# Kernel optimization log

Measured on AMD Instinct MI355X. Metric: run time of the kernel, lower is better.

## Reference

```python
import jax, jax.numpy as jnp
import numpy as np

N0, N1, N2, DEG = 100000, 50000, 25000, 16
IN, HID, OUT = 256, 128, 128
H1, H2 = 2, 1
E1, E2 = N1 * DEG, N2 * DEG


def setup_inputs() -> dict:
    key = jax.random.key(0)
    ks = jax.random.split(key, 16)
    x = jax.random.normal(ks[0], (N0, IN), dtype=jnp.float32)
    # neighbor-sampled bipartite edges: each dst node has DEG sampled src neighbors
    row1 = jnp.repeat(jnp.arange(N1, dtype=jnp.int32), DEG)
    col1 = jax.random.randint(ks[1], (E1,), 0, N0, dtype=jnp.int32)
    t1 = jax.random.randint(ks[2], (E1,), 0, 100, dtype=jnp.int32)
    row2 = jnp.repeat(jnp.arange(N2, dtype=jnp.int32), DEG)
    col2 = jax.random.randint(ks[3], (E2,), 0, N1, dtype=jnp.int32)
    t2 = jax.random.randint(ks[4], (E2,), 0, 100, dtype=jnp.int32)
    s_in = 1.0 / np.sqrt(IN)
    s_h = 1.0 / np.sqrt(HID)
    s_bn = 1.0 / np.sqrt(HID * H1)
    return dict(
        x=x, row1=row1, col1=col1, t1=t1, row2=row2, col2=col2, t2=t2,
        time=10, interval=20,
        Ws1=jax.random.normal(ks[5], (IN, H1 * HID), jnp.float32) * s_in,
        Wd1=jax.random.normal(ks[6], (IN, H1 * HID), jnp.float32) * s_in,
        as1=jax.random.normal(ks[7], (H1, HID), jnp.float32) * s_h,
        ad1=jax.random.normal(ks[8], (H1, HID), jnp.float32) * s_h,
        b1=jnp.zeros((H1 * HID,), jnp.float32),
        g1=jnp.ones((H1 * HID,), jnp.float32),
        beta1=jnp.zeros((H1 * HID,), jnp.float32),
        m1=jnp.zeros((H1 * HID,), jnp.float32),
        v1=jnp.ones((H1 * HID,), jnp.float32),
        Ws2=jax.random.normal(ks[9], (H1 * HID, H2 * OUT), jnp.float32) * s_bn,
        Wd2=jax.random.normal(ks[10], (H1 * HID, H2 * OUT), jnp.float32) * s_bn,
        as2=jax.random.normal(ks[11], (H2, OUT), jnp.float32) * s_h,
        ad2=jax.random.normal(ks[12], (H2, OUT), jnp.float32) * s_h,
        b2=jnp.zeros((H2 * OUT,), jnp.float32),
    )


def gat_conv(hs, hd, row, col, mask, att_s, att_d, n_dst):
    # hs: [Ns,H,C] transformed src feats, hd: [Nd,H,C]; row=dst idx, col=src idx per edge
    a_s = jnp.sum(hs * att_s, axis=-1)  # [Ns,H]
    a_d = jnp.sum(hd * att_d, axis=-1)  # [Nd,H]
    e = jax.nn.leaky_relu(a_s[col] + a_d[row], negative_slope=0.2)  # [E,H]
    e = jnp.where(mask[:, None], e, -jnp.inf)
    m = jax.ops.segment_max(e, row, num_segments=n_dst)  # [Nd,H]
    m = jnp.where(jnp.isfinite(m), m, 0.0)
    ex = jnp.where(mask[:, None], jnp.exp(e - m[row]), 0.0)
    denom = jax.ops.segment_sum(ex, row, num_segments=n_dst)
    alpha = ex / jnp.maximum(denom[row], 1e-16)  # edge softmax over incoming edges
    out = jax.ops.segment_sum(alpha[:, :, None] * hs[col], row, num_segments=n_dst)
    return out  # [Nd,H,C]


def _forward(x, Ws1, Wd1, as1, ad1, b1, g1, beta1, m1, v1,
             Ws2, Wd2, as2, ad2, b2,
             row1, col1, t1, row2, col2, t2, time, interval):
    # temporal edge masking: keep edges with timestamp in [time, time+interval)
    mask1 = (t1 >= time) & (t1 < time + interval)
    mask2 = (t2 >= time) & (t2 < time + interval)
    # ---- layer 1: GATConv(IN -> HID, heads=H1, concat=True) ----
    hs = (x @ Ws1).reshape(N0, H1, HID)
    hd = (x[:N1] @ Wd1).reshape(N1, H1, HID)
    h = gat_conv(hs, hd, row1, col1, mask1, as1, ad1, N1).reshape(N1, H1 * HID) + b1
    # BatchNorm1d (eval: running stats), then leaky_relu (slope 0.01); dropout off (eval)
    h = (h - m1) * jax.lax.rsqrt(v1 + 1e-5) * g1 + beta1
    h = jax.nn.leaky_relu(h, negative_slope=0.01)
    # ---- layer 2: GATConv(H1*HID -> OUT, heads=H2, concat=False) ----
    hs2 = (h @ Ws2).reshape(N1, H2, OUT)
    hd2 = (h[:N2] @ Wd2).reshape(N2, H2, OUT)
    out = gat_conv(hs2, hd2, row2, col2, mask2, as2, ad2, N2)
    out = jnp.mean(out, axis=1) + b2  # concat=False -> mean over heads
    return out  # [N2, OUT]


def reference(x, row1, col1, t1, row2, col2, t2, time, interval,
              Ws1, Wd1, as1, ad1, b1, g1, beta1, m1, v1,
              Ws2, Wd2, as2, ad2, b2):
    return _forward(x, Ws1, Wd1, as1, ad1, b1, g1, beta1, m1, v1,
                    Ws2, Wd2, as2, ad2, b2,
                    row1, col1, t1, row2, col2, t2, time, interval)
```

## Files before the change

kernel.cpp:

```cpp
#include <hip/hip_runtime.h>
#include <hip/hip_bf16.h>

#define N0C 100000
#define N1C 50000
#define N2C 25000

typedef _Float16 f16;
typedef _Float16 f16x2 __attribute__((ext_vector_type(2)));
typedef _Float16 f16x4 __attribute__((ext_vector_type(4)));
typedef _Float16 f16x8 __attribute__((ext_vector_type(8)));
typedef float f32x16 __attribute__((ext_vector_type(16)));

typedef const __attribute__((address_space(1))) unsigned int guint;
typedef __attribute__((address_space(3))) unsigned int luint;
__device__ __forceinline__ void gload16(const void* g, void* l) {
    __builtin_amdgcn_global_load_lds((guint*)g, (luint*)l, 16, 0, 0);
}

__device__ __forceinline__ f16x8 cvt8(float4 a, float4 b) {
    return (f16x8){(f16)a.x, (f16)a.y, (f16)a.z, (f16)a.w,
                   (f16)b.x, (f16)b.y, (f16)b.z, (f16)b.w};
}

__global__ void prep1_kernel(const float* __restrict__ Ws1, const float* __restrict__ Wd1,
                             const float* __restrict__ as1, const float* __restrict__ ad1,
                             const float* __restrict__ Ws2, const float* __restrict__ Wd2,
                             const float* __restrict__ as2, const float* __restrict__ ad2,
                             const float* __restrict__ b1, const float* __restrict__ g1,
                             const float* __restrict__ beta1, const float* __restrict__ m1,
                             const float* __restrict__ v1,
                             float* __restrict__ e1, float* __restrict__ e2,
                             float* __restrict__ bns, float* __restrict__ bnt) {
    int k = blockIdx.x, lane = threadIdx.x;
    float s0 = 0, s1 = 0, d0 = 0, d1 = 0, t0 = 0, t1 = 0;
    for (int c = lane; c < 128; c += 64) {
        s0 += Ws1[k * 256 + c] * as1[c];
        s1 += Ws1[k * 256 + 128 + c] * as1[128 + c];
        d0 += Wd1[k * 256 + c] * ad1[c];
        d1 += Wd1[k * 256 + 128 + c] * ad1[128 + c];
        t0 += Ws2[k * 128 + c] * as2[c];
        t1 += Wd2[k * 128 + c] * ad2[c];
    }
    for (int d = 1; d < 64; d <<= 1) {
        s0 += __shfl_xor(s0, d); s1 += __shfl_xor(s1, d);
        d0 += __shfl_xor(d0, d); d1 += __shfl_xor(d1, d);
        t0 += __shfl_xor(t0, d); t1 += __shfl_xor(t1, d);
    }
    if (lane == 0) {
        e1[k * 4 + 0] = s0; e1[k * 4 + 1] = s1; e1[k * 4 + 2] = d0; e1[k * 4 + 3] = d1;
        e2[k * 2 + 0] = t0; e2[k * 2 + 1] = t1;
        float sc = g1[k] * rsqrtf(v1[k] + 1e-5f);
        bns[k] = sc;
        bnt[k] = (b1[k] - m1[k]) * sc + beta1[k];
    }
}

__global__ void prep2_kernel(const float* __restrict__ Ws1, const float* __restrict__ Ws2,
                             const float* __restrict__ e1, const float* __restrict__ e2,
                             f16* __restrict__ bfl1, f16* __restrict__ bfl2) {
    int i = blockIdx.x * 256 + threadIdx.x;
    if (i < 73728) {
        int j = i & 7, lane = (i >> 3) & 63, kb = (i >> 9) & 15, nt = i >> 13;
        int c = lane & 31, hi = lane >> 5;
        int k = kb * 16 + hi * 8 + j;
        float v;
        if (nt < 8) v = Ws1[k * 256 + nt * 32 + c];
        else v = (c < 4) ? e1[k * 4 + c] : 0.f;
        bfl1[i] = (f16)v;
    } else {
        int i2 = i - 73728;
        if (i2 < 40960) {
            int j = i2 & 7, lane = (i2 >> 3) & 63, kb = (i2 >> 9) & 15, nt = i2 >> 13;
            int c = lane & 31, hi = lane >> 5;
            int k = kb * 16 + hi * 8 + j;
            float v;
            if (nt < 4) v = Ws2[k * 128 + nt * 32 + c];
            else v = (c < 2) ? e2[k * 2 + c] : 0.f;
            bfl2[i2] = (f16)v;
        }
    }
}

__global__ __launch_bounds__(384, 8) void gemm1_kernel(
    const float* __restrict__ x, const f16* __restrict__ bfl,
    f16* __restrict__ hs, float* __restrict__ as_out, float* __restrict__ ad_out) {
    __shared__ __align__(16) unsigned char smA[16384];
    const int t = threadIdx.x;
    const int wave = t >> 6, lane = t & 63;
    const int ntl = wave >> 1, khalf = wave & 1;
    const int nt = blockIdx.y * 3 + ntl;
    const int col = lane & 31, hi = lane >> 5;
    const int r0 = blockIdx.x * 32;

    if (t < 256) {
        const float4* xs = (const float4*)(x + (size_t)r0 * 256);
#pragma unroll
        for (int p = 0; p < 4; p++) {
            int i = t + 256 * p;
            float4 a0 = xs[i * 2], a1 = xs[i * 2 + 1];
            int row = i >> 5, c = i & 31;
            *(f16x8*)(smA + row * 512 + (c ^ (row & 7)) * 16) = cvt8(a0, a1);
        }
    }
    f16x8 b[8];
#pragma unroll
    for (int i = 0; i < 8; i++)
        b[i] = *(const f16x8*)(bfl + ((size_t)(nt * 16 + khalf * 8 + i) * 64 + lane) * 8);

    __syncthreads();
    const int r7 = col & 7;
    f32x16 acc = {};
#pragma unroll
    for (int i = 0; i < 8; i++) {
        int kb = khalf * 8 + i;
        int sl = (2 * kb + hi) ^ r7;
        f16x8 af = *(const f16x8*)(smA + col * 512 + sl * 16);
        acc = __builtin_amdgcn_mfma_f32_32x32x16_f16(af, b[i], acc, 0, 0, 0);
    }
    __syncthreads();
    if (khalf == 1) {
        float* rb = (float*)(smA + ntl * 4096) + lane * 16;
#pragma unroll
        for (int r = 0; r < 16; r++) rb[r] = acc[r];
    }
    __syncthreads();
    if (khalf == 0) {
        const float* rb = (const float*)(smA + ntl * 4096) + lane * 16;
        if (nt < 8) {
#pragma unroll
            for (int r = 0; r < 16; r++) {
                int grow = r0 + (r & 3) + 8 * (r >> 2) + 4 * hi;
                hs[(size_t)grow * 256 + nt * 32 + col] = (f16)(acc[r] + rb[r]);
            }
        } else {
#pragma unroll
            for (int r = 0; r < 16; r++) {
                int grow = r0 + (r & 3) + 8 * (r >> 2) + 4 * hi;
                float v = acc[r] + rb[r];
                if (col < 2) {
                    as_out[grow * 2 + col] = v;
                } else if (col < 4) {
                    if (grow < N1C) ad_out[grow * 2 + (col - 2)] = v;
                }
            }
        }
    }
}

__global__ __launch_bounds__(640, 8) void gemm2_kernel(
    const f16* __restrict__ h, const f16* __restrict__ bfl,
    f16* __restrict__ hs2, float* __restrict__ as_out, float* __restrict__ ad_out) {
    __shared__ __align__(16) unsigned char smA[20480];
    const int t = threadIdx.x;
    const int wave = t >> 6, lane = t & 63;
    const int ntl = wave >> 1, khalf = wave & 1;
    const int col = lane & 31, hi = lane >> 5;
    const int r0 = blockIdx.x * 32;

    if (t < 256) {
#pragma unroll
        for (int p = 0; p < 4; p++) {
            int i = p * 256 + t;
            int row = i >> 5, s = i & 31;
            int grow = r0 + row;
            if (grow > N1C - 1) grow = N1C - 1;
            const f16* src = h + (size_t)grow * 256 + ((s ^ (row & 7)) * 8);
            gload16(src, smA + p * 4096 + (t >> 6) * 1024 + (lane << 4));
        }
    }
    f16x8 b[8];
#pragma unroll
    for (int i = 0; i < 8; i++)
        b[i] = *(const f16x8*)(bfl + ((size_t)(ntl * 16 + khalf * 8 + i) * 64 + lane) * 8);

    __syncthreads();
    const int r7 = col & 7;
    f32x16 acc = {};
#pragma unroll
    for (int i = 0; i < 8; i++) {
        int kb = khalf * 8 + i;
        int sl = (2 * kb + hi) ^ r7;
        f16x8 af = *(const f16x8*)(smA + col * 512 + sl * 16);
        acc = __builtin_amdgcn_mfma_f32_32x32x16_f16(af, b[i], acc, 0, 0, 0);
    }
    __syncthreads();
    if (khalf == 1) {
        float* rb = (float*)(smA + ntl * 4096) + lane * 16;
#pragma unroll
        for (int r = 0; r < 16; r++) rb[r] = acc[r];
    }
    __syncthreads();
    if (khalf == 0) {
        const float* rb = (const float*)(smA + ntl * 4096) + lane * 16;
        if (ntl < 4) {
#pragma unroll
            for (int r = 0; r < 16; r++) {
                int grow = r0 + (r & 3) + 8 * (r >> 2) + 4 * hi;
                if (grow < N1C) hs2[(size_t)grow * 128 + ntl * 32 + col] = (f16)(acc[r] + rb[r]);
            }
        } else {
#pragma unroll
            for (int r = 0; r < 16; r++) {
                int grow = r0 + (r & 3) + 8 * (r >> 2) + 4 * hi;
                float v = acc[r] + rb[r];
                if (col == 0) {
                    if (grow < N1C) as_out[grow] = v;
                } else if (col == 1) {
                    if (grow < N2C) ad_out[grow] = v;
                }
            }
        }
    }
}

__global__ void agg1_kernel(const int* __restrict__ col1, const int* __restrict__ t1,
                            const int* __restrict__ timep, const int* __restrict__ intervalp,
                            const float* __restrict__ a_s, const float* __restrict__ a_d,
                            const f16* __restrict__ hs,
                            const float* __restrict__ bns, const float* __restrict__ bnt,
                            f16* __restrict__ h) {
    int wid = (blockIdx.x * blockDim.x + threadIdx.x) >> 6;
    if (wid >= N1C) return;
    int lane = threadIdx.x & 63;
    int T = timep[0], I = intervalp[0];
    int j = lane & 15;
    int c = col1[wid * 16 + j];
    int tv = t1[wid * 16 + j];
    bool mk = (tv >= T) && (tv < T + I);
    float e0 = -INFINITY, e1 = -INFINITY;
    if (mk) {
        float s0 = a_s[c * 2 + 0] + a_d[wid * 2 + 0];
        float s1 = a_s[c * 2 + 1] + a_d[wid * 2 + 1];
        e0 = s0 > 0.f ? s0 : 0.2f * s0;
        e1 = s1 > 0.f ? s1 : 0.2f * s1;
    }
    float m0 = e0, m1 = e1;
#pragma unroll
    for (int d = 1; d < 16; d <<= 1) {
        m0 = fmaxf(m0, __shfl_xor(m0, d));
        m1 = fmaxf(m1, __shfl_xor(m1, d));
    }
    float ex0 = mk ? __expf(e0 - m0) : 0.f;
    float ex1 = mk ? __expf(e1 - m1) : 0.f;
    float s0 = ex0, s1 = ex1;
#pragma unroll
    for (int d = 1; d < 16; d <<= 1) {
        s0 += __shfl_xor(s0, d);
        s1 += __shfl_xor(s1, d);
    }
    float r0 = 1.f / fmaxf(s0, 1e-16f);
    float r1 = 1.f / fmaxf(s1, 1e-16f);
    unsigned long long mb = __ballot(mk) & 0xFFFFull;
    int head = lane >> 5;
    float rden = head ? r1 : r0;
    float acc0 = 0.f, acc1 = 0.f, acc2 = 0.f, acc3 = 0.f;
    while (mb) {
        int jj = __builtin_ctzll(mb);
        mb &= mb - 1;
        int cj = __shfl(c, jj);
        float w0 = __shfl(ex0, jj), w1 = __shfl(ex1, jj);
        float w = (head ? w1 : w0) * rden;
        f16x4 v = *(const f16x4*)(hs + (size_t)cj * 256 + lane * 4);
        acc0 += w * (float)v[0];
        acc1 += w * (float)v[1];
        acc2 += w * (float)v[2];
        acc3 += w * (float)v[3];
    }
    int cb = lane * 4;
    float4 sc = *(const float4*)(bns + cb);
    float4 sh = *(const float4*)(bnt + cb);
    float o0 = acc0 * sc.x + sh.x; o0 = o0 > 0.f ? o0 : 0.01f * o0;
    float o1 = acc1 * sc.y + sh.y; o1 = o1 > 0.f ? o1 : 0.01f * o1;
    float o2 = acc2 * sc.z + sh.z; o2 = o2 > 0.f ? o2 : 0.01f * o2;
    float o3 = acc3 * sc.w + sh.w; o3 = o3 > 0.f ? o3 : 0.01f * o3;
    f16x4 ov = {(f16)o0, (f16)o1, (f16)o2, (f16)o3};
    *(f16x4*)(h + (size_t)wid * 256 + cb) = ov;
}

__global__ void agg2_kernel(const int* __restrict__ col2, const int* __restrict__ t2,
                            const int* __restrict__ timep, const int* __restrict__ intervalp,
                            const float* __restrict__ a_s, const float* __restrict__ a_d,
                            const f16* __restrict__ hs2,
                            const float* __restrict__ b2, float* __restrict__ out) {
    int wid = (blockIdx.x * blockDim.x + threadIdx.x) >> 6;
    if (wid >= N2C) return;
    int lane = threadIdx.x & 63;
    int T = timep[0], I = intervalp[0];
    int j = lane & 15;
    int c = col2[wid * 16 + j];
    int tv = t2[wid * 16 + j];
    bool mk = (tv >= T) && (tv < T + I);
    float e = -INFINITY;
    if (mk) {
        float s = a_s[c] + a_d[wid];
        e = s > 0.f ? s : 0.2f * s;
    }
    float m = e;
#pragma unroll
    for (int d = 1; d < 16; d <<= 1) m = fmaxf(m, __shfl_xor(m, d));
    float ex = mk ? __expf(e - m) : 0.f;
    float s = ex;
#pragma unroll
    for (int d = 1; d < 16; d <<= 1) s += __shfl_xor(s, d);
    float r = 1.f / fmaxf(s, 1e-16f);
    unsigned long long mb = __ballot(mk) & 0xFFFFull;
    float acc0 = 0.f, acc1 = 0.f;
    while (mb) {
        int jj = __builtin_ctzll(mb);
        mb &= mb - 1;
        int cj = __shfl(c, jj);
        float w = __shfl(ex, jj) * r;
        f16x2 v = *(const f16x2*)(hs2 + (size_t)cj * 128 + lane * 2);
        acc0 += w * (float)v[0];
        acc1 += w * (float)v[1];
    }
    float2 o = make_float2(acc0 + b2[lane * 2], acc1 + b2[lane * 2 + 1]);
    *(float2*)(out + (size_t)wid * 128 + lane * 2) = o;
}

extern "C" void kernel_launch(void* const* d_in, const int* in_sizes, int n_in,
                              void* d_out, int out_size, void* d_ws, size_t ws_size,
                              hipStream_t stream) {
    const float* x = (const float*)d_in[0];
    const int* col1 = (const int*)d_in[2];
    const int* t1 = (const int*)d_in[3];
    const int* col2 = (const int*)d_in[5];
    const int* t2 = (const int*)d_in[6];
    const int* timep = (const int*)d_in[7];
    const int* intervalp = (const int*)d_in[8];
    const float* Ws1 = (const float*)d_in[9];
    const float* Wd1 = (const float*)d_in[10];
    const float* as1 = (const float*)d_in[11];
    const float* ad1 = (const float*)d_in[12];
    const float* b1 = (const float*)d_in[13];
    const float* g1 = (const float*)d_in[14];
    const float* beta1 = (const float*)d_in[15];
    const float* m1 = (const float*)d_in[16];
    const float* v1 = (const float*)d_in[17];
    const float* Ws2 = (const float*)d_in[18];
    const float* Wd2 = (const float*)d_in[19];
    const float* as2 = (const float*)d_in[20];
    const float* ad2 = (const float*)d_in[21];
    const float* b2 = (const float*)d_in[22];
    float* out = (float*)d_out;

    char* ws = (char*)d_ws;
    size_t off = 0;
    auto alloc = [&](size_t bytes) {
        size_t o = off;
        off += (bytes + 511) & ~(size_t)511;
        return o;
    };
    f16* hs = (f16*)(ws + alloc((size_t)N0C * 256 * 2));
    f16* h = (f16*)(ws + alloc((size_t)N1C * 256 * 2));
    f16* hs2 = (f16*)(ws + alloc((size_t)N1C * 128 * 2));
    float* a_s1 = (float*)(ws + alloc((size_t)N0C * 2 * 4));
    float* a_d1 = (float*)(ws + alloc((size_t)N1C * 2 * 4));
    float* a_s2 = (float*)(ws + alloc((size_t)N1C * 4));
    float* a_d2 = (float*)(ws + alloc((size_t)N2C * 4));
    f16* bfl1 = (f16*)(ws + alloc((size_t)73728 * 2));
    f16* bfl2 = (f16*)(ws + alloc((size_t)40960 * 2));
    float* e1 = (float*)(ws + alloc(1024 * 4));
    float* e2 = (float*)(ws + alloc(512 * 4));
    float* bns = (float*)(ws + alloc(256 * 4));
    float* bnt = (float*)(ws + alloc(256 * 4));

    prep1_kernel<<<256, 64, 0, stream>>>(Ws1, Wd1, as1, ad1, Ws2, Wd2, as2, ad2,
                                         b1, g1, beta1, m1, v1, e1, e2, bns, bnt);
    prep2_kernel<<<448, 256, 0, stream>>>(Ws1, Ws2, e1, e2, bfl1, bfl2);
    gemm1_kernel<<<dim3(3125, 3), 384, 0, stream>>>(x, bfl1, hs, a_s1, a_d1);
    agg1_kernel<<<N1C / 4, 256, 0, stream>>>(col1, t1, timep, intervalp,
                                             a_s1, a_d1, hs, bns, bnt, h);
    gemm2_kernel<<<(N1C + 31) / 32, 640, 0, stream>>>(h, bfl2, hs2, a_s2, a_d2);
    agg2_kernel<<<N2C / 4, 256, 0, stream>>>(col2, t2, timep, intervalp,
                                             a_s2, a_d2, hs2, b2, out);
}
```

Baseline: 123.0 us.

## Make gemm1 persistent with double-buffered x tiles and register-resident weights

Layer-1 GEMM becomes a persistent kernel of 512 blocks by 512 threads. Each block loops over 32-row tiles of x and prefetches the next tile into a second LDS buffer while the current one is computed. Each wave keeps its full K=256 column-tile of weights in registers, so the k-split reduction through LDS goes away and x is read once instead of three times across grid.y. Wave 0 also computes the attention-logit projection from weights staged in LDS, which gives it roughly double the MFMA work of the other waves and may cause imbalance and register pressure.

```diff
diff --git a/kernel.cpp b/kernel.cpp
--- a/kernel.cpp
+++ b/kernel.cpp
@@ -81,69 +81,89 @@
     }
 }
 
-__global__ __launch_bounds__(384, 8) void gemm1_kernel(
+__global__ __launch_bounds__(512, 4) void gemm1_kernel(
     const float* __restrict__ x, const f16* __restrict__ bfl,
     f16* __restrict__ hs, float* __restrict__ as_out, float* __restrict__ ad_out) {
-    __shared__ __align__(16) unsigned char smA[16384];
+    __shared__ __align__(16) unsigned char smA[2][16384];
+    __shared__ __align__(16) unsigned char smP[16384];
     const int t = threadIdx.x;
     const int wave = t >> 6, lane = t & 63;
-    const int ntl = wave >> 1, khalf = wave & 1;
-    const int nt = blockIdx.y * 3 + ntl;
     const int col = lane & 31, hi = lane >> 5;
-    const int r0 = blockIdx.x * 32;
-
-    if (t < 256) {
-        const float4* xs = (const float4*)(x + (size_t)r0 * 256);
-#pragma unroll
-        for (int p = 0; p < 4; p++) {
-            int i = t + 256 * p;
-            float4 a0 = xs[i * 2], a1 = xs[i * 2 + 1];
-            int row = i >> 5, c = i & 31;
-            *(f16x8*)(smA + row * 512 + (c ^ (row & 7)) * 16) = cvt8(a0, a1);
-        }
-    }
-    f16x8 b[8];
-#pragma unroll
-    for (int i = 0; i < 8; i++)
-        b[i] = *(const f16x8*)(bfl + ((size_t)(nt * 16 + khalf * 8 + i) * 64 + lane) * 8);
-
+    const int nt = wave;
+
+    f16x8 b[16];
+#pragma unroll
+    for (int kb = 0; kb < 16; kb++)
+        b[kb] = *(const f16x8*)(bfl + ((size_t)(nt * 16 + kb) * 64 + lane) * 8);
+
+    {
+        int c0 = wave * 2;
+        gload16(bfl + ((size_t)(8 * 16 + c0) * 64 + lane) * 8, smP + (c0 * 64 + lane) * 16);
+        gload16(bfl + ((size_t)(8 * 16 + c0 + 1) * 64 + lane) * 8, smP + ((c0 + 1) * 64 + lane) * 16);
+    }
+
+    const int srow = t >> 4, sseg = t & 15;
+    const int c2 = sseg * 2, r7s = srow & 7;
+    const int t0 = blockIdx.x;
+    {
+        const float4* p = (const float4*)(x + ((size_t)t0 * 32 + srow) * 256 + sseg * 16);
+        float4 a0 = p[0], a1 = p[1], a2 = p[2], a3 = p[3];
+        unsigned char* wb = smA[0] + srow * 512;
+        *(f16x8*)(wb + ((c2 ^ r7s) * 16)) = cvt8(a0, a1);
+        *(f16x8*)(wb + (((c2 + 1) ^ r7s) * 16)) = cvt8(a2, a3);
+    }
     __syncthreads();
-    const int r7 = col & 7;
-    f32x16 acc = {};
-#pragma unroll
-    for (int i = 0; i < 8; i++) {
-        int kb = khalf * 8 + i;
-        int sl = (2 * kb + hi) ^ r7;
-        f16x8 af = *(const f16x8*)(smA + col * 512 + sl * 16);
-        acc = __builtin_amdgcn_mfma_f32_32x32x16_f16(af, b[i], acc, 0, 0, 0);
-    }
-    __syncthreads();
-    if (khalf == 1) {
-        float* rb = (float*)(smA + ntl * 4096) + lane * 16;
-#pragma unroll
-        for (int r = 0; r < 16; r++) rb[r] = acc[r];
-    }
-    __syncthreads();
-    if (khalf == 0) {
-        const float* rb = (const float*)(smA + ntl * 4096) + lane * 16;
-        if (nt < 8) {
+
+    int cur = 0;
+    for (int tt = t0; tt < 3125; tt += 512) {
+        const bool pre = (tt + 512) < 3125;
+        float4 a0, a1, a2, a3;
+        if (pre) {
+            const float4* p = (const float4*)(x + ((size_t)(tt + 512) * 32 + srow) * 256 + sseg * 16);
+            a0 = p[0]; a1 = p[1]; a2 = p[2]; a3 = p[3];
+        }
+        const unsigned char* buf = smA[cur];
+        const int r0 = tt * 32;
+        if (wave == 0) {
+            f32x16 acc = {}, accp = {};
+#pragma unroll
+            for (int kb = 0; kb < 16; kb++) {
+                f16x8 af = *(const f16x8*)(buf + col * 512 + (((2 * kb + hi) ^ (col & 7)) * 16));
+                f16x8 bp = *(const f16x8*)(smP + (kb * 64 + lane) * 16);
+                acc = __builtin_amdgcn_mfma_f32_32x32x16_f16(af, b[kb], acc, 0, 0, 0);
+                accp = __builtin_amdgcn_mfma_f32_32x32x16_f16(af, bp, accp, 0, 0, 0);
+            }
 #pragma unroll
             for (int r = 0; r < 16; r++) {
                 int grow = r0 + (r & 3) + 8 * (r >> 2) + 4 * hi;
-                hs[(size_t)grow * 256 + nt * 32 + col] = (f16)(acc[r] + rb[r]);
-            }
-        } else {
-#pragma unroll
-            for (int r = 0; r < 16; r++) {
-                int grow = r0 + (r & 3) + 8 * (r >> 2) + 4 * hi;
-                float v = acc[r] + rb[r];
+                hs[(size_t)grow * 256 + col] = (f16)acc[r];
+                float v = accp[r];
                 if (col < 2) {
                     as_out[grow * 2 + col] = v;
                 } else if (col < 4) {
                     if (grow < N1C) ad_out[grow * 2 + (col - 2)] = v;
                 }
             }
-        }
+        } else {
+            f32x16 acc = {};
+#pragma unroll
+            for (int kb = 0; kb < 16; kb++) {
+                f16x8 af = *(const f16x8*)(buf + col * 512 + (((2 * kb + hi) ^ (col & 7)) * 16));
+                acc = __builtin_amdgcn_mfma_f32_32x32x16_f16(af, b[kb], acc, 0, 0, 0);
+            }
+#pragma unroll
+            for (int r = 0; r < 16; r++) {
+                int grow = r0 + (r & 3) + 8 * (r >> 2) + 4 * hi;
+                hs[(size_t)grow * 256 + nt * 32 + col] = (f16)acc[r];
+            }
+        }
+        if (pre) {
+            unsigned char* wb = smA[cur ^ 1] + srow * 512;
+            *(f16x8*)(wb + ((c2 ^ r7s) * 16)) = cvt8(a0, a1);
+            *(f16x8*)(wb + (((c2 + 1) ^ r7s) * 16)) = cvt8(a2, a3);
+        }
+        __syncthreads();
+        cur ^= 1;
     }
 }
 
@@ -368,7 +388,7 @@
     prep1_kernel<<<256, 64, 0, stream>>>(Ws1, Wd1, as1, ad1, Ws2, Wd2, as2, ad2,
                                          b1, g1, beta1, m1, v1, e1, e2, bns, bnt);
     prep2_kernel<<<448, 256, 0, stream>>>(Ws1, Ws2, e1, e2, bfl1, bfl2);
-    gemm1_kernel<<<dim3(3125, 3), 384, 0, stream>>>(x, bfl1, hs, a_s1, a_d1);
+    gemm1_kernel<<<512, 512, 0, stream>>>(x, bfl1, hs, a_s1, a_d1);
     agg1_kernel<<<N1C / 4, 256, 0, stream>>>(col1, t1, timep, intervalp,
                                              a_s1, a_d1, hs, bns, bnt, h);
     gemm2_kernel<<<(N1C + 31) / 32, 640, 0, stream>>>(h, bfl2, hs2, a_s2, a_d2);
```

New measurement: 179.3 us. +45.8%, slower.
